# Kernel tuning notes

Measured on AMD Instinct MI355X. Metric: run time of the kernel, lower is better.

The kernel has to match this reference:

```python
import jax, jax.numpy as jnp
import numpy as np

D = 128  # feature_dim

def setup_inputs() -> dict:
    key = jax.random.key(0)
    ks = jax.random.split(key, 10)
    B, Sq, Skv = 32, 2048, 2048
    scale = 1.0 / np.sqrt(D)
    inp = {
        'smiles_features': jax.random.normal(ks[0], (B, Skv, D), jnp.float32),
        'image_features': jax.random.normal(ks[1], (B, Sq, D), jnp.float32),
        'Wv': jax.random.normal(ks[2], (D, D), jnp.float32) * scale,
        'bv': jnp.zeros((D,), jnp.float32),
        'Wk': jax.random.normal(ks[3], (D, D), jnp.float32) * scale,
        'bk': jnp.zeros((D,), jnp.float32),
        'Wq': jax.random.normal(ks[4], (D, D), jnp.float32) * scale,
        'bq': jnp.zeros((D,), jnp.float32),
        'Wd': jax.random.normal(ks[5], (D, D), jnp.float32) * scale,
        'bd': jnp.zeros((D,), jnp.float32),
    }
    return inp

def reference(smiles_features, image_features, Wv, bv, Wk, bk, Wq, bq, Wd, bd):
    # Linear layers: y = x @ W^T + b (torch convention)
    V = smiles_features @ Wv.T + bv          # [B, Skv, D]
    K = smiles_features @ Wk.T + bk          # [B, Skv, D]
    Q = image_features @ Wq.T + bq           # [B, Sq, D]
    # energy = Q K^T / sqrt(128) (hard-coded 128 in original)
    energy = jnp.einsum('bqd,bkd->bqk', Q, K) / jnp.sqrt(jnp.float32(128.0))
    attention = jax.nn.softmax(energy, axis=-1)
    fusion = jnp.einsum('bqk,bkd->bqd', attention, V)
    output = fusion @ Wd.T + bd
    return output
```

## Files before the change

kernel.cpp:

```cpp
#include <hip/hip_runtime.h>
#include <hip/hip_bf16.h>

typedef __attribute__((ext_vector_type(4))) float f32x4;
typedef __attribute__((ext_vector_type(16))) float f32x16;
typedef __attribute__((ext_vector_type(8))) short bf16x8;
typedef __attribute__((ext_vector_type(4))) unsigned int uint4v;
typedef __attribute__((ext_vector_type(2))) unsigned int uint2v;

#define MFMA16(a, b, c) __builtin_amdgcn_mfma_f32_16x16x32_bf16(a, b, c, 0, 0, 0)
#define MFMA32(a, b, c) __builtin_amdgcn_mfma_f32_32x32x16_bf16(a, b, c, 0, 0, 0)

__device__ __forceinline__ unsigned short f2bf(float f) {
  union { float f; unsigned u; } v; v.f = f;
  unsigned r = v.u + 0x7fffu + ((v.u >> 16) & 1u);
  return (unsigned short)(r >> 16);
}
__device__ __forceinline__ unsigned pack2(float a, float b) {
  union { __hip_bfloat162 h2; unsigned u; } cv;
  cv.h2 = __hip_bfloat162(__float2bfloat16(a), __float2bfloat16(b));
  return cv.u;
}

__device__ __forceinline__ void swap32(unsigned a, unsigned b, int hi,
                                       unsigned& ox, unsigned& oy) {
#if __has_builtin(__builtin_amdgcn_permlane32_swap)
  uint2v r = __builtin_amdgcn_permlane32_swap(a, b, false, false);
  ox = r[0]; oy = r[1];
#else
  unsigned sb = __shfl_xor(b, 32);
  unsigned sa = __shfl_xor(a, 32);
  ox = hi ? sb : a;
  oy = hi ? b : sa;
#endif
}

template<bool IN_F32, int OUT_MODE>
__global__ __launch_bounds__(256)
void proj_kernel(const void* __restrict__ xin, const float* __restrict__ W,
                 const float* __restrict__ bias, void* __restrict__ yout,
                 float scale)
{
  __shared__ __align__(16) unsigned short Ws[128][136];
  __shared__ __align__(16) unsigned short Xs[64][136];
  const int t = threadIdx.x;
  const int wid = t >> 6;
  const int lane = t & 63;
  const int ln = lane & 15, g = lane >> 4;
  const long row0 = (long)blockIdx.x * 64;

  float bz[8];
#pragma unroll
  for (int tt = 0; tt < 8; ++tt) bz[tt] = bias[tt * 16 + ln];

#pragma unroll
  for (int i = 0; i < 16; ++i) {
    int idx = (i * 256 + t) * 4;
    int r = idx >> 7, c = idx & 127;
    const float4 w4 = *reinterpret_cast<const float4*>(W + idx);
    ushort4 wb;
    wb.x = f2bf(w4.x); wb.y = f2bf(w4.y); wb.z = f2bf(w4.z); wb.w = f2bf(w4.w);
    *reinterpret_cast<ushort4*>(&Ws[r][c]) = wb;
  }
  if (IN_F32) {
    const float* x = (const float*)xin;
#pragma unroll
    for (int i = 0; i < 8; ++i) {
      int idx = (i * 256 + t) * 4;
      int r = idx >> 7, c = idx & 127;
      const float4 x4 = *reinterpret_cast<const float4*>(x + row0 * 128 + idx);
      ushort4 xb;
      xb.x = f2bf(x4.x); xb.y = f2bf(x4.y); xb.z = f2bf(x4.z); xb.w = f2bf(x4.w);
      *reinterpret_cast<ushort4*>(&Xs[r][c]) = xb;
    }
  } else {
    const unsigned short* x = (const unsigned short*)xin;
#pragma unroll
    for (int i = 0; i < 4; ++i) {
      int idx = (i * 256 + t) * 8;
      int r = idx >> 7, c = idx & 127;
      *reinterpret_cast<uint4v*>(&Xs[r][c]) =
          *reinterpret_cast<const uint4v*>(x + row0 * 128 + idx);
    }
  }
  __syncthreads();

  f32x4 acc[8];
#pragma unroll
  for (int tt = 0; tt < 8; ++tt) acc[tt] = (f32x4){0.f, 0.f, 0.f, 0.f};

#pragma unroll
  for (int c = 0; c < 4; ++c) {
    bf16x8 af = *reinterpret_cast<const bf16x8*>(&Xs[wid * 16 + ln][c * 32 + g * 8]);
#pragma unroll
    for (int tt = 0; tt < 8; ++tt) {
      bf16x8 bfr = *reinterpret_cast<const bf16x8*>(&Ws[tt * 16 + ln][c * 32 + g * 8]);
      acc[tt] = MFMA16(af, bfr, acc[tt]);
    }
  }

#pragma unroll
  for (int tt = 0; tt < 8; ++tt) {
#pragma unroll
    for (int r = 0; r < 4; ++r) {
      long row = row0 + wid * 16 + g * 4 + r;
      int col = tt * 16 + ln;
      float val = (acc[tt][r] + bz[tt]) * scale;
      if (OUT_MODE == 2) {
        ((float*)yout)[row * 128 + col] = val;
      } else if (OUT_MODE == 0) {
        ((unsigned short*)yout)[row * 128 + col] = f2bf(val);
      } else {
        long bb = row >> 11, rr = row & 2047;
        ((unsigned short*)yout)[(bb * 128 + col) * 2048 + rr] = f2bf(val);
      }
    }
  }
}

__global__ __launch_bounds__(256)
void attn_kernel(const unsigned short* __restrict__ Qg,
                 const unsigned short* __restrict__ Kg,
                 const unsigned short* __restrict__ Vtg,
                 unsigned short* __restrict__ Fg)
{
  __shared__ __align__(16) unsigned short Ks[32][136];
  __shared__ __align__(16) unsigned short Vs[128][40];

  const int t = threadIdx.x;
  const int lane = t & 63;
  const int q = lane & 31;
  const int hi = lane >> 5;
  const int wid = t >> 6;
  const int b = blockIdx.y;
  const int q0 = blockIdx.x * 128 + wid * 32;

  const unsigned short* Qb = Qg + (long)b * 2048 * 128;
  const unsigned short* Kb = Kg + (long)b * 2048 * 128;
  const unsigned short* Vb = Vtg + (long)b * 128 * 2048;

  const int kr = t >> 4, kc = (t & 15) * 8;
  const int vc = t >> 2, ko = (t & 3) * 8;

  bf16x8 qf[8];
#pragma unroll
  for (int c = 0; c < 8; ++c)
    qf[c] = *reinterpret_cast<const bf16x8*>(
        Qb + (long)(q0 + q) * 128 + c * 16 + hi * 8);

  f32x16 o[4];
#pragma unroll
  for (int dc = 0; dc < 4; ++dc)
#pragma unroll
    for (int r = 0; r < 16; ++r) o[dc][r] = 0.f;
  float mrun = -1e30f;
  float lrun = 0.f;

  uint4v kreg0 = *reinterpret_cast<const uint4v*>(Kb + (long)kr * 128 + kc);
  uint4v kreg1 = *reinterpret_cast<const uint4v*>(Kb + (long)(kr + 16) * 128 + kc);
  uint4v vreg0 = *reinterpret_cast<const uint4v*>(Vb + (long)vc * 2048 + ko);
  uint4v vreg1 = *reinterpret_cast<const uint4v*>(Vb + (long)(vc + 64) * 2048 + ko);

  for (int kt = 0; kt < 64; ++kt) {
    __syncthreads();
    *reinterpret_cast<uint4v*>(&Ks[kr][kc]) = kreg0;
    *reinterpret_cast<uint4v*>(&Ks[kr + 16][kc]) = kreg1;
    *reinterpret_cast<uint4v*>(&Vs[vc][ko]) = vreg0;
    *reinterpret_cast<uint4v*>(&Vs[vc + 64][ko]) = vreg1;
    __syncthreads();

    if (kt < 63) {
      const int nv0 = (kt + 1) * 32;
      kreg0 = *reinterpret_cast<const uint4v*>(Kb + (long)(nv0 + kr) * 128 + kc);
      kreg1 = *reinterpret_cast<const uint4v*>(Kb + (long)(nv0 + kr + 16) * 128 + kc);
      vreg0 = *reinterpret_cast<const uint4v*>(Vb + (long)vc * 2048 + nv0 + ko);
      vreg1 = *reinterpret_cast<const uint4v*>(Vb + (long)(vc + 64) * 2048 + nv0 + ko);
    }

    f32x16 st;
#pragma unroll
    for (int r = 0; r < 16; ++r) st[r] = 0.f;
    __builtin_amdgcn_s_setprio(1);
#pragma unroll
    for (int c = 0; c < 8; ++c) {
      bf16x8 kf = *reinterpret_cast<const bf16x8*>(&Ks[q][c * 16 + hi * 8]);
      st = MFMA32(kf, qf[c], st);
    }
    __builtin_amdgcn_s_setprio(0);

    float tm = st[0];
#pragma unroll
    for (int r = 1; r < 16; ++r) tm = fmaxf(tm, st[r]);
    tm = fmaxf(tm, __shfl_xor(tm, 32));

    float mcur = mrun;
    if (!__all(tm <= mcur + 8.0f)) {
      float mnew = fmaxf(mcur, tm);
      float al = __builtin_amdgcn_exp2f(mcur - mnew);
      mrun = mnew;
      mcur = mnew;
      lrun *= al;
#pragma unroll
      for (int r = 0; r < 16; ++r) {
        float ar = __shfl(al, (r & 3) + 8 * (r >> 2) + 4 * hi);
#pragma unroll
        for (int dc = 0; dc < 4; ++dc) o[dc][r] *= ar;
      }
    }

    unsigned pk[8];
    float s[8];
#pragma unroll
    for (int j = 0; j < 8; ++j) {
      float pa_ = __builtin_amdgcn_exp2f(st[2 * j] - mcur);
      float pb_ = __builtin_amdgcn_exp2f(st[2 * j + 1] - mcur);
      s[j] = pa_ + pb_;
      pk[j] = pack2(pa_, pb_);
    }
#pragma unroll
    for (int j = 0; j < 4; ++j) s[j] += s[j + 4];
    lrun += (s[0] + s[1]) + (s[2] + s[3]);

    union { unsigned u[4]; bf16x8 v; } pa0, pa1;
    swap32(pk[0], pk[2], hi, pa0.u[0], pa0.u[2]);
    swap32(pk[1], pk[3], hi, pa0.u[1], pa0.u[3]);
    swap32(pk[4], pk[6], hi, pa1.u[0], pa1.u[2]);
    swap32(pk[5], pk[7], hi, pa1.u[1], pa1.u[3]);

    __builtin_amdgcn_s_setprio(1);
#pragma unroll
    for (int dc = 0; dc < 4; ++dc) {
      bf16x8 vf0 = *reinterpret_cast<const bf16x8*>(&Vs[dc * 32 + q][hi * 8]);
      bf16x8 vf1 = *reinterpret_cast<const bf16x8*>(&Vs[dc * 32 + q][16 + hi * 8]);
      o[dc] = MFMA32(pa0.v, vf0, o[dc]);
      o[dc] = MFMA32(pa1.v, vf1, o[dc]);
    }
    __builtin_amdgcn_s_setprio(0);
  }

  float ltot = lrun + __shfl_xor(lrun, 32);
  float inv = 1.f / ltot;
#pragma unroll
  for (int r = 0; r < 16; ++r) {
    const int qr = (r & 3) + 8 * (r >> 2) + 4 * hi;
    float invr = __shfl(inv, qr);
    long row = (long)b * 2048 + q0 + qr;
#pragma unroll
    for (int dc = 0; dc < 4; ++dc)
      Fg[row * 128 + dc * 32 + q] = f2bf(o[dc][r] * invr);
  }
}

extern "C" void kernel_launch(void* const* d_in, const int* in_sizes, int n_in,
                              void* d_out, int out_size, void* d_ws, size_t ws_size,
                              hipStream_t stream)
{
  (void)in_sizes; (void)n_in; (void)out_size; (void)ws_size;
  const float* smiles = (const float*)d_in[0];
  const float* image  = (const float*)d_in[1];
  const float* Wv = (const float*)d_in[2]; const float* bv = (const float*)d_in[3];
  const float* Wk = (const float*)d_in[4]; const float* bk = (const float*)d_in[5];
  const float* Wq = (const float*)d_in[6]; const float* bq = (const float*)d_in[7];
  const float* Wd = (const float*)d_in[8]; const float* bd = (const float*)d_in[9];

  unsigned short* Qw = (unsigned short*)d_ws;
  unsigned short* Kw = Qw + 8388608;
  unsigned short* Vw = Kw + 8388608;
  unsigned short* Fw = Vw + 8388608;

  const float qscale = 1.4426950408889634f * 0.08838834764831845f;

  dim3 blk(256);
  proj_kernel<true, 0><<<dim3(1024), blk, 0, stream>>>(image,  Wq, bq, Qw, qscale);
  proj_kernel<true, 0><<<dim3(1024), blk, 0, stream>>>(smiles, Wk, bk, Kw, 1.f);
  proj_kernel<true, 1><<<dim3(1024), blk, 0, stream>>>(smiles, Wv, bv, Vw, 1.f);
  attn_kernel<<<dim3(16, 32), blk, 0, stream>>>(Qw, Kw, Vw, Fw);
  proj_kernel<false, 2><<<dim3(1024), blk, 0, stream>>>(Fw, Wd, bd, (float*)d_out, 1.f);
}
```

Before: 132.6 us.

## Fuse K and V projections into one kernel and remap attention blocks for XCD locality

Adds a kernel that loads each smiles tile once, converts it to bf16, and computes both the K and V projections. This removes one kernel launch and a second full read of the fp32 smiles input. The attention grid becomes 1D with a remapped block index, so that consecutive block IDs modulo 8 land on different batches. The apparent aim is to keep each batch's K/V within one XCD's L2. The fused kernel reloads W through LDS between the two GEMMs, adding extra syncs.

```diff
diff --git a/kernel.cpp b/kernel.cpp
--- a/kernel.cpp
+++ b/kernel.cpp
@@ -118,6 +118,98 @@
 }
 
 __global__ __launch_bounds__(256)
+void proj_kv_kernel(const float* __restrict__ x,
+                    const float* __restrict__ Wk, const float* __restrict__ bk,
+                    const float* __restrict__ Wv, const float* __restrict__ bv,
+                    unsigned short* __restrict__ Kout,
+                    unsigned short* __restrict__ Vout)
+{
+  __shared__ __align__(16) unsigned short Ws[128][136];
+  __shared__ __align__(16) unsigned short Xs[64][136];
+  const int t = threadIdx.x;
+  const int wid = t >> 6;
+  const int lane = t & 63;
+  const int ln = lane & 15, g = lane >> 4;
+  const long row0 = (long)blockIdx.x * 64;
+
+  float bzk[8], bzv[8];
+#pragma unroll
+  for (int tt = 0; tt < 8; ++tt) { bzk[tt] = bk[tt * 16 + ln]; bzv[tt] = bv[tt * 16 + ln]; }
+
+#pragma unroll
+  for (int i = 0; i < 8; ++i) {
+    int idx = (i * 256 + t) * 4;
+    int r = idx >> 7, c = idx & 127;
+    const float4 x4 = *reinterpret_cast<const float4*>(x + row0 * 128 + idx);
+    ushort4 xb;
+    xb.x = f2bf(x4.x); xb.y = f2bf(x4.y); xb.z = f2bf(x4.z); xb.w = f2bf(x4.w);
+    *reinterpret_cast<ushort4*>(&Xs[r][c]) = xb;
+  }
+#pragma unroll
+  for (int i = 0; i < 16; ++i) {
+    int idx = (i * 256 + t) * 4;
+    int r = idx >> 7, c = idx & 127;
+    const float4 w4 = *reinterpret_cast<const float4*>(Wk + idx);
+    ushort4 wb;
+    wb.x = f2bf(w4.x); wb.y = f2bf(w4.y); wb.z = f2bf(w4.z); wb.w = f2bf(w4.w);
+    *reinterpret_cast<ushort4*>(&Ws[r][c]) = wb;
+  }
+  __syncthreads();
+
+  f32x4 acc[8];
+#pragma unroll
+  for (int tt = 0; tt < 8; ++tt) acc[tt] = (f32x4){0.f, 0.f, 0.f, 0.f};
+#pragma unroll
+  for (int c = 0; c < 4; ++c) {
+    bf16x8 af = *reinterpret_cast<const bf16x8*>(&Xs[wid * 16 + ln][c * 32 + g * 8]);
+#pragma unroll
+    for (int tt = 0; tt < 8; ++tt) {
+      bf16x8 bfr = *reinterpret_cast<const bf16x8*>(&Ws[tt * 16 + ln][c * 32 + g * 8]);
+      acc[tt] = MFMA16(af, bfr, acc[tt]);
+    }
+  }
+#pragma unroll
+  for (int tt = 0; tt < 8; ++tt)
+#pragma unroll
+    for (int r = 0; r < 4; ++r) {
+      long row = row0 + wid * 16 + g * 4 + r;
+      Kout[row * 128 + tt * 16 + ln] = f2bf(acc[tt][r] + bzk[tt]);
+    }
+
+  __syncthreads();
+#pragma unroll
+  for (int i = 0; i < 16; ++i) {
+    int idx = (i * 256 + t) * 4;
+    int r = idx >> 7, c = idx & 127;
+    const float4 w4 = *reinterpret_cast<const float4*>(Wv + idx);
+    ushort4 wb;
+    wb.x = f2bf(w4.x); wb.y = f2bf(w4.y); wb.z = f2bf(w4.z); wb.w = f2bf(w4.w);
+    *reinterpret_cast<ushort4*>(&Ws[r][c]) = wb;
+  }
+  __syncthreads();
+
+#pragma unroll
+  for (int tt = 0; tt < 8; ++tt) acc[tt] = (f32x4){0.f, 0.f, 0.f, 0.f};
+#pragma unroll
+  for (int c = 0; c < 4; ++c) {
+    bf16x8 af = *reinterpret_cast<const bf16x8*>(&Xs[wid * 16 + ln][c * 32 + g * 8]);
+#pragma unroll
+    for (int tt = 0; tt < 8; ++tt) {
+      bf16x8 bfr = *reinterpret_cast<const bf16x8*>(&Ws[tt * 16 + ln][c * 32 + g * 8]);
+      acc[tt] = MFMA16(af, bfr, acc[tt]);
+    }
+  }
+#pragma unroll
+  for (int tt = 0; tt < 8; ++tt)
+#pragma unroll
+    for (int r = 0; r < 4; ++r) {
+      long row = row0 + wid * 16 + g * 4 + r;
+      long bb = row >> 11, rr = row & 2047;
+      Vout[(bb * 128 + tt * 16 + ln) * 2048 + rr] = f2bf(acc[tt][r] + bzv[tt]);
+    }
+}
+
+__global__ __launch_bounds__(256)
 void attn_kernel(const unsigned short* __restrict__ Qg,
                  const unsigned short* __restrict__ Kg,
                  const unsigned short* __restrict__ Vtg,
@@ -131,8 +223,12 @@
   const int q = lane & 31;
   const int hi = lane >> 5;
   const int wid = t >> 6;
-  const int b = blockIdx.y;
-  const int q0 = blockIdx.x * 128 + wid * 32;
+
+  const int gbid = blockIdx.x;
+  const int k_ = gbid >> 3, r_ = gbid & 7;
+  const int b = r_ + 8 * (k_ >> 4);
+  const int j = k_ & 15;
+  const int q0 = j * 128 + wid * 32;
 
   const unsigned short* Qb = Qg + (long)b * 2048 * 128;
   const unsigned short* Kb = Kg + (long)b * 2048 * 128;
@@ -210,14 +306,14 @@
     unsigned pk[8];
     float s[8];
 #pragma unroll
-    for (int j = 0; j < 8; ++j) {
-      float pa_ = __builtin_amdgcn_exp2f(st[2 * j] - mcur);
-      float pb_ = __builtin_amdgcn_exp2f(st[2 * j + 1] - mcur);
-      s[j] = pa_ + pb_;
-      pk[j] = pack2(pa_, pb_);
-    }
-#pragma unroll
-    for (int j = 0; j < 4; ++j) s[j] += s[j + 4];
+    for (int j2 = 0; j2 < 8; ++j2) {
+      float pa_ = __builtin_amdgcn_exp2f(st[2 * j2] - mcur);
+      float pb_ = __builtin_amdgcn_exp2f(st[2 * j2 + 1] - mcur);
+      s[j2] = pa_ + pb_;
+      pk[j2] = pack2(pa_, pb_);
+    }
+#pragma unroll
+    for (int j2 = 0; j2 < 4; ++j2) s[j2] += s[j2 + 4];
     lrun += (s[0] + s[1]) + (s[2] + s[3]);
 
     union { unsigned u[4]; bf16x8 v; } pa0, pa1;
@@ -270,9 +366,8 @@
   const float qscale = 1.4426950408889634f * 0.08838834764831845f;
 
   dim3 blk(256);
-  proj_kernel<true, 0><<<dim3(1024), blk, 0, stream>>>(image,  Wq, bq, Qw, qscale);
-  proj_kernel<true, 0><<<dim3(1024), blk, 0, stream>>>(smiles, Wk, bk, Kw, 1.f);
-  proj_kernel<true, 1><<<dim3(1024), blk, 0, stream>>>(smiles, Wv, bv, Vw, 1.f);
-  attn_kernel<<<dim3(16, 32), blk, 0, stream>>>(Qw, Kw, Vw, Fw);
+  proj_kernel<true, 0><<<dim3(1024), blk, 0, stream>>>(image, Wq, bq, Qw, qscale);
+  proj_kv_kernel<<<dim3(1024), blk, 0, stream>>>(smiles, Wk, bk, Wv, bv, Kw, Vw);
+  attn_kernel<<<dim3(512), blk, 0, stream>>>(Qw, Kw, Vw, Fw);
   proj_kernel<false, 2><<<dim3(1024), blk, 0, stream>>>(Fw, Wd, bd, (float*)d_out, 1.f);
 }
```

New measurement: 128.1 us. -3.4%, faster.
